# Kernel optimization log

Measured on AMD Instinct MI355X. Metric: run time of the kernel, lower is better.

The kernel has to match this reference:

```python
import jax, jax.numpy as jnp
import numpy as np

B, N, E = 128, 256, 2048
BINS = 16

def _gcn(x, src, dst, W, b):
    # GCNConv with self-loops and symmetric deg^-1/2 normalization (PyG default).
    h = x @ W  # [N, Fout]
    deg = jnp.zeros(x.shape[0], x.dtype).at[dst].add(1.0) + 1.0  # +1 self-loop
    dinv = jax.lax.rsqrt(deg)
    coef = dinv[src] * dinv[dst]  # [E]
    agg = jnp.zeros_like(h).at[dst].add(h[src] * coef[:, None])
    return agg + h / deg[:, None] + b  # self-loop norm = 1/deg

def _gnn(x, ei, W1, b1, W2, b2, W3, b3):
    # x: [B,N,Fin], ei: [B,2,E]. Dropout skipped (eval mode).
    def single(x, ei):
        s, d = ei[0], ei[1]
        h = jax.nn.relu(_gcn(x, s, d, W1, b1))
        h = jax.nn.relu(_gcn(h, s, d, W2, b2))
        return _gcn(h, s, d, W3, b3)
    return jax.vmap(single)(x, ei)

def _att_pool(x, Watt):
    # SimGNN attention pooling; all graphs have exactly N nodes.
    ctx = jnp.tanh((x @ Watt.T).sum(axis=1) / jnp.asarray(N, x.dtype))  # [B,f3]
    scores = jax.nn.sigmoid(jnp.einsum('bnf,bf->bn', x, ctx))  # [B,N]
    return jnp.einsum('bnf,bn->bf', x, scores)  # [B,f3]

def _forward(xq, xc, eq, ec, W1, b1, W2, b2, W3, b3, Watt, ntnW, ntnV, ntnb, fc1W, fc1b, fc2W, fc2b):
    q = _gnn(xq, eq, W1, b1, W2, b2, W3, b3)  # [B,N,f3]
    c = _gnn(xc, ec, W1, b1, W2, b2, W3, b3)
    e1 = _att_pool(q, Watt)
    e2 = _att_pool(c, Watt)
    # NTN: bilinear + linear on concat + bias
    scores = jax.nn.relu(
        jnp.einsum('bi,tij,bj->bt', e1, ntnW, e2)
        + jnp.concatenate([e1, e2], axis=-1) @ ntnV.T
        + ntnb
    )  # [B, tensor_neurons]
    # histogram of all pairwise node-embedding dot products (torch.histc semantics)
    s = jnp.einsum('bnf,bmf->bnm', q, c).ravel()
    lo, hi = s.min(), s.max()
    idx = jnp.clip(jnp.floor((s - lo) / (hi - lo) * BINS).astype(jnp.int32), 0, BINS - 1)
    counts = jnp.zeros(BINS, s.dtype).at[idx].add(1.0)
    h = jax.lax.stop_gradient(counts / counts.sum())
    scores = jnp.concatenate([scores, jnp.broadcast_to(h, (scores.shape[0], BINS))], axis=1)
    scores = jax.nn.relu(scores @ fc1W.T + fc1b)
    p = jax.nn.sigmoid(scores @ fc2W.T + fc2b)  # [B,1]
    return p.squeeze()


def setup_inputs() -> dict:
    key = jax.random.key(0)
    ks = jax.random.split(key, 20)
    Fin, f1, f2, f3, T, BN = 128, 128, 64, 32, 16, 16
    def xav(k, shape):
        fan_in, fan_out = shape[-1], shape[0]
        lim = np.sqrt(6.0 / (fan_in + fan_out))
        return jax.random.uniform(k, shape, jnp.float32, -lim, lim)
    return {
        'xq': jax.random.normal(ks[0], (B, N, Fin), jnp.float32),
        'xc': jax.random.normal(ks[1], (B, N, Fin), jnp.float32),
        'eq': jax.random.randint(ks[2], (B, 2, E), 0, N, jnp.int32),
        'ec': jax.random.randint(ks[3], (B, 2, E), 0, N, jnp.int32),
        'W1': xav(ks[4], (Fin, f1)), 'b1': jnp.zeros((f1,), jnp.float32),
        'W2': xav(ks[5], (f1, f2)), 'b2': jnp.zeros((f2,), jnp.float32),
        'W3': xav(ks[6], (f2, f3)), 'b3': jnp.zeros((f3,), jnp.float32),
        'Watt': xav(ks[7], (f3, f3)),
        'ntnW': xav(ks[8], (T, f3, f3)),
        'ntnV': xav(ks[9], (T, 2 * f3)),
        'ntnb': xav(ks[10], (T, 1)).squeeze(-1),
        'fc1W': xav(ks[11], (BN, T + BINS)), 'fc1b': jnp.zeros((BN,), jnp.float32),
        'fc2W': xav(ks[12], (1, BN)), 'fc2b': jnp.zeros((1,), jnp.float32),
    }


def reference(xq, xc, eq, ec, W1, b1, W2, b2, W3, b3, Watt, ntnW, ntnV, ntnb, fc1W, fc1b, fc2W, fc2b):
    return _forward(xq, xc, eq, ec, W1, b1, W2, b2, W3, b3, Watt, ntnW, ntnV, ntnb, fc1W, fc1b, fc2W, fc2b)
```

## Files before the change

kernel.cpp:

```cpp
#include <hip/hip_runtime.h>
#include <math.h>

#define BB 128
#define NN 256
#define EE 2048
#define BINS 16

typedef unsigned short u16;

__global__ void csr_kernel(const int* __restrict__ eq, const int* __restrict__ ec,
                           int* __restrict__ off, u16* __restrict__ srcs,
                           float* __restrict__ dvsg) {
    int g = blockIdx.x;
    int b = g < BB ? g : g - BB;
    const int* ei = g < BB ? eq : ec;
    int t = threadIdx.x;
    __shared__ int cnt[NN];
    __shared__ int sa[NN], sb[NN];
    __shared__ int cursor[NN];
    cnt[t] = 0;
    __syncthreads();
    const int* src = ei + b * 2 * EE;
    const int* dst = src + EE;
    for (int e = t; e < EE; e += 256) atomicAdd(&cnt[dst[e]], 1);
    __syncthreads();
    dvsg[g * NN + t] = rsqrtf((float)cnt[t] + 1.0f);
    sa[t] = cnt[t];
    __syncthreads();
    int* pin = sa; int* pout = sb;
    for (int d = 1; d < NN; d <<= 1) {
        int v = pin[t];
        if (t >= d) v += pin[t - d];
        pout[t] = v;
        __syncthreads();
        int* tmp = pin; pin = pout; pout = tmp;
    }
    int excl = pin[t] - cnt[t];
    off[g * 257 + t] = excl;
    if (t == 255) off[g * 257 + 256] = EE;
    cursor[t] = excl;
    __syncthreads();
    for (int e = t; e < EE; e += 256) {
        int d = dst[e], s = src[e];
        int pos = atomicAdd(&cursor[d], 1);
        srcs[g * EE + pos] = (u16)s;
    }
}

template<int FIN, int FOUT, bool RELU, int NSPLIT>
__global__ __launch_bounds__(512) void gcn_fused4(
        const float* __restrict__ X0, const float* __restrict__ X1,
        const float* __restrict__ W, const float* __restrict__ bias,
        const int* __restrict__ off, const u16* __restrict__ srcs,
        const float* __restrict__ dvsg, float* __restrict__ OUT) {
    constexpr int CHUNKS = FOUT / 32;
    int blk = blockIdx.x;
    int g = blk % (2 * BB);
    int rest = blk / (2 * BB);
    int cb = (rest % CHUNKS) * 32;
    int half = rest / CHUNKS;
    int t = threadIdx.x;

    __shared__ float uni[NN * 33];
    __shared__ int   eoff[NN + 1];
    __shared__ u16   esrc[EE];
    __shared__ float dvs_s[NN];
    float* xsT = uni;
    float* wt  = uni + 16 * 260;
    float* hT  = uni;

    const float* xg = (g < BB) ? (X0 + (size_t)g * NN * FIN)
                               : (X1 + (size_t)(g - BB) * NN * FIN);
    const int* o = off + g * 257;
    const u16* sr = srcs + (size_t)g * EE;

    for (int i = t; i < EE; i += 512) esrc[i] = sr[i];
    for (int i = t; i <= NN; i += 512) eoff[i] = o[i];
    if (t < NN) dvs_s[t] = dvsg[g * NN + t];

    int l = t & 63;
    int wv = t >> 6;

    float acc[4][4];
#pragma unroll
    for (int i = 0; i < 4; i++)
#pragma unroll
        for (int j = 0; j < 4; j++) acc[i][j] = 0.f;

    int sn = t >> 1, qk = (t & 1) * 8;
    const float* xr = xg + sn * FIN + qk;
    float4 v0 = *(const float4*)xr;
    float4 v1 = *(const float4*)(xr + 4);
    float wreg = W[(t >> 5) * FOUT + cb + (t & 31)];

    for (int k0 = 0; k0 < FIN; k0 += 16) {
        xsT[(qk + 0) * 260 + sn] = v0.x;
        xsT[(qk + 1) * 260 + sn] = v0.y;
        xsT[(qk + 2) * 260 + sn] = v0.z;
        xsT[(qk + 3) * 260 + sn] = v0.w;
        xsT[(qk + 4) * 260 + sn] = v1.x;
        xsT[(qk + 5) * 260 + sn] = v1.y;
        xsT[(qk + 6) * 260 + sn] = v1.z;
        xsT[(qk + 7) * 260 + sn] = v1.w;
        wt[t] = wreg;
        __syncthreads();
        if (k0 + 16 < FIN) {
            xr += 16;
            v0 = *(const float4*)xr;
            v1 = *(const float4*)(xr + 4);
            wreg = W[(k0 + 16 + (t >> 5)) * FOUT + cb + (t & 31)];
        }
#pragma unroll
        for (int k = 0; k < 16; k++) {
            float4 xv = *(const float4*)&xsT[k * 260 + 4 * l];
            float4 wvv = *(const float4*)&wt[k * 32 + 4 * wv];
            acc[0][0] += xv.x * wvv.x; acc[0][1] += xv.x * wvv.y;
            acc[0][2] += xv.x * wvv.z; acc[0][3] += xv.x * wvv.w;
            acc[1][0] += xv.y * wvv.x; acc[1][1] += xv.y * wvv.y;
            acc[1][2] += xv.y * wvv.z; acc[1][3] += xv.y * wvv.w;
            acc[2][0] += xv.z * wvv.x; acc[2][1] += xv.z * wvv.y;
            acc[2][2] += xv.z * wvv.z; acc[2][3] += xv.z * wvv.w;
            acc[3][0] += xv.w * wvv.x; acc[3][1] += xv.w * wvv.y;
            acc[3][2] += xv.w * wvv.z; acc[3][3] += xv.w * wvv.w;
        }
        __syncthreads();
    }
#pragma unroll
    for (int i = 0; i < 4; i++)
#pragma unroll
        for (int j = 0; j < 4; j++)
            hT[(4 * l + i) * 33 + 4 * wv + j] = acc[i][j];
    __syncthreads();

    int c = t & 31, ng = t >> 5;
    float bb_ = bias[cb + c];
    float* outp = OUT + (size_t)g * NN * FOUT;
    constexpr int NSEG = NN / NSPLIT;
    int nlo = half * NSEG, nhi = nlo + NSEG;
    for (int n = nlo + ng; n < nhi; n += 16) {
        int j0 = eoff[n], j1 = eoff[n + 1];
        float dn = dvs_s[n];
        float a = 0.f;
        int j = j0;
        for (; j + 1 < j1; j += 2) {
            int s0 = esrc[j], s1 = esrc[j + 1];
            a += hT[s0 * 33 + c] * (dvs_s[s0] * dn);
            a += hT[s1 * 33 + c] * (dvs_s[s1] * dn);
        }
        if (j < j1) {
            int s0 = esrc[j];
            a += hT[s0 * 33 + c] * (dvs_s[s0] * dn);
        }
        float d0i = 1.0f / ((float)(j1 - j0) + 1.0f);
        float val = a + hT[n * 33 + c] * d0i + bb_;
        if (RELU) val = fmaxf(val, 0.f);
        outp[n * FOUT + cb + c] = val;
    }
}

__global__ void attpool_kernel(const float* __restrict__ X, const float* __restrict__ Watt,
                               float* __restrict__ e) {
    int g = blockIdx.x;
    int t = threadIdx.x;
    __shared__ float xs[NN * 33];
    __shared__ float red[256];
    __shared__ float mean_s[32], ctx_s[32], sc[NN];
    const float* x = X + (size_t)g * NN * 32;
    for (int i = t; i < NN * 32; i += 256) { int n = i >> 5, c = i & 31; xs[n * 33 + c] = x[i]; }
    __syncthreads();
    {
        int c = t & 31, p = t >> 5;
        float s = 0.f;
        for (int n = p * 32; n < (p + 1) * 32; n++) s += xs[n * 33 + c];
        red[t] = s;
    }
    __syncthreads();
    if (t < 32) {
        float m = 0.f;
        for (int p = 0; p < 8; p++) m += red[p * 32 + t];
        mean_s[t] = m / (float)NN;
    }
    __syncthreads();
    if (t < 32) {
        float a = 0.f;
        for (int f = 0; f < 32; f++) a += mean_s[f] * Watt[t * 32 + f];
        ctx_s[t] = tanhf(a);
    }
    __syncthreads();
    {
        float a = 0.f;
        for (int f = 0; f < 32; f++) a += xs[t * 33 + f] * ctx_s[f];
        sc[t] = 1.f / (1.f + expf(-a));
    }
    __syncthreads();
    {
        int c = t & 31, p = t >> 5;
        float s = 0.f;
        for (int n = p * 32; n < (p + 1) * 32; n++) s += xs[n * 33 + c] * sc[n];
        red[t] = s;
    }
    __syncthreads();
    if (t < 32) {
        float s = 0.f;
        for (int p = 0; p < 8; p++) s += red[p * 32 + t];
        e[g * 32 + t] = s;
    }
}

#define PD_STAGE_AND_DOT \
    int blk = blockIdx.x; \
    int b = blk >> 2; \
    int tq = (blk >> 1) & 1, tc = blk & 1; \
    __shared__ float qsT[32 * 132]; \
    __shared__ float csT[32 * 132]; \
    int t = threadIdx.x; \
    { \
        int n = t >> 1, f0 = (t & 1) * 16; \
        const float* qp = Q + ((size_t)b * NN + tq * 128 + n) * 32 + f0; \
        const float* cp = C + ((size_t)b * NN + tc * 128 + n) * 32 + f0; \
        float qa16[16], ca16[16]; \
        *(float4*)&qa16[0]  = *(const float4*)(qp); \
        *(float4*)&qa16[4]  = *(const float4*)(qp + 4); \
        *(float4*)&qa16[8]  = *(const float4*)(qp + 8); \
        *(float4*)&qa16[12] = *(const float4*)(qp + 12); \
        *(float4*)&ca16[0]  = *(const float4*)(cp); \
        *(float4*)&ca16[4]  = *(const float4*)(cp + 4); \
        *(float4*)&ca16[8]  = *(const float4*)(cp + 8); \
        *(float4*)&ca16[12] = *(const float4*)(cp + 12); \
        _Pragma("unroll") \
        for (int m = 0; m < 16; m++) { \
            qsT[(f0 + m) * 132 + n] = qa16[m]; \
            csT[(f0 + m) * 132 + n] = ca16[m]; \
        } \
    } \
    __syncthreads(); \
    int rg = (t >> 4) * 4, cg = (t & 15) * 4; \
    float acc[8][8]; \
    _Pragma("unroll") \
    for (int i = 0; i < 8; i++) \
        _Pragma("unroll") \
        for (int j = 0; j < 8; j++) acc[i][j] = 0.f; \
    _Pragma("unroll 2") \
    for (int f = 0; f < 32; f++) { \
        float4 qa = *(const float4*)&qsT[f * 132 + rg]; \
        float4 qb = *(const float4*)&qsT[f * 132 + 64 + rg]; \
        float4 ca = *(const float4*)&csT[f * 132 + cg]; \
        float4 cb = *(const float4*)&csT[f * 132 + 64 + cg]; \
        float qv[8] = {qa.x, qa.y, qa.z, qa.w, qb.x, qb.y, qb.z, qb.w}; \
        float cv[8] = {ca.x, ca.y, ca.z, ca.w, cb.x, cb.y, cb.z, cb.w}; \
        _Pragma("unroll") \
        for (int i = 0; i < 8; i++) \
            _Pragma("unroll") \
            for (int j = 0; j < 8; j++) acc[i][j] += qv[i] * cv[j]; \
    }

__global__ __launch_bounds__(256, 4) void pairdot_minmax(
        const float* __restrict__ Q, const float* __restrict__ C,
        float* __restrict__ bmin, float* __restrict__ bmax) {
    PD_STAGE_AND_DOT
    float lmin = acc[0][0], lmax = acc[0][0];
#pragma unroll
    for (int i = 0; i < 8; i++)
#pragma unroll
        for (int j = 0; j < 8; j++) {
            lmin = fminf(lmin, acc[i][j]);
            lmax = fmaxf(lmax, acc[i][j]);
        }
    __shared__ float rmin[256], rmax[256];
    rmin[t] = lmin; rmax[t] = lmax;
    __syncthreads();
    for (int s = 128; s > 0; s >>= 1) {
        if (t < s) { rmin[t] = fminf(rmin[t], rmin[t + s]); rmax[t] = fmaxf(rmax[t], rmax[t + s]); }
        __syncthreads();
    }
    if (t == 0) { bmin[blk] = rmin[0]; bmax[blk] = rmax[0]; }
}

__global__ void minmax_kernel(const float* __restrict__ bmin, const float* __restrict__ bmax,
                              float* __restrict__ lohi, float* __restrict__ counts) {
    __shared__ float rmin[256], rmax[256];
    int t = threadIdx.x;
    float lmin = 1e30f, lmax = -1e30f;
    for (int i = t; i < 512; i += 256) { lmin = fminf(lmin, bmin[i]); lmax = fmaxf(lmax, bmax[i]); }
    rmin[t] = lmin; rmax[t] = lmax;
    __syncthreads();
    for (int s = 128; s > 0; s >>= 1) {
        if (t < s) { rmin[t] = fminf(rmin[t], rmin[t + s]); rmax[t] = fmaxf(rmax[t], rmax[t + s]); }
        __syncthreads();
    }
    if (t == 0) { lohi[0] = rmin[0]; lohi[1] = rmax[0]; }
    if (t < BINS) counts[t] = 0.f;
}

__global__ __launch_bounds__(256, 4) void pairdot_hist(
        const float* __restrict__ Q, const float* __restrict__ C,
        const float* __restrict__ lohi, float* __restrict__ counts) {
    PD_STAGE_AND_DOT
    float lo = lohi[0], hi = lohi[1];
    float scale = (float)BINS / (hi - lo);
    int lane = t & 63;
    int cnt = 0;
#pragma unroll
    for (int i = 0; i < 8; i++)
#pragma unroll
        for (int j = 0; j < 8; j++) {
            int idx = (int)floorf((acc[i][j] - lo) * scale);
            idx = min(max(idx, 0), BINS - 1);
            unsigned long long b0 = __ballot((idx & 1) != 0);
            unsigned long long b1 = __ballot((idx & 2) != 0);
            unsigned long long b2 = __ballot((idx & 4) != 0);
            unsigned long long b3 = __ballot((idx & 8) != 0);
            unsigned long long msk = ((lane & 1) ? b0 : ~b0);
            msk &= ((lane & 2) ? b1 : ~b1);
            msk &= ((lane & 4) ? b2 : ~b2);
            msk &= ((lane & 8) ? b3 : ~b3);
            cnt += __popcll(msk);
        }
    __shared__ float wbins[4][BINS];
    int wave = t >> 6;
    if (lane < BINS) wbins[wave][lane] = (float)cnt;
    __syncthreads();
    if (t < BINS) {
        atomicAdd(&counts[t], wbins[0][t] + wbins[1][t] + wbins[2][t] + wbins[3][t]);
    }
}

__global__ void final_kernel(const float* __restrict__ e1, const float* __restrict__ e2,
                             const float* __restrict__ ntnW, const float* __restrict__ ntnV,
                             const float* __restrict__ ntnb, const float* __restrict__ counts,
                             const float* __restrict__ fc1W, const float* __restrict__ fc1b,
                             const float* __restrict__ fc2W, const float* __restrict__ fc2b,
                             float* __restrict__ out) {
    int b = blockIdx.x;
    int t = threadIdx.x;
    __shared__ float a1[32], a2[32], red[256], z[32], u[16];
    if (t < 32) a1[t] = e1[b * 32 + t];
    else if (t < 64) a2[t - 32] = e2[b * 32 + t - 32];
    __syncthreads();
    int tt = t >> 4, g = t & 15;
    float p = 0.f;
#pragma unroll
    for (int ii = 0; ii < 2; ii++) {
        int i = g + 16 * ii;
        float d = 0.f;
        const float* wr = ntnW + (tt * 32 + i) * 32;
        for (int j = 0; j < 32; j++) d += wr[j] * a2[j];
        p += a1[i] * d;
    }
    red[t] = p;
    __syncthreads();
    if (t < 16) {
        float s = 0.f;
        for (int g2 = 0; g2 < 16; g2++) s += red[t * 16 + g2];
        float lin = ntnb[t];
        for (int i = 0; i < 32; i++) lin += ntnV[t * 64 + i] * a1[i];
        for (int i = 0; i < 32; i++) lin += ntnV[t * 64 + 32 + i] * a2[i];
        z[t] = fmaxf(s + lin, 0.f);
    } else if (t < 32) {
        float tot = 0.f;
        for (int i = 0; i < BINS; i++) tot += counts[i];
        z[t] = counts[t - 16] / tot;
    }
    __syncthreads();
    if (t < 16) {
        float a = fc1b[t];
        for (int i = 0; i < 32; i++) a += fc1W[t * 32 + i] * z[i];
        u[t] = fmaxf(a, 0.f);
    }
    __syncthreads();
    if (t == 0) {
        float a = fc2b[0];
        for (int i = 0; i < 16; i++) a += fc2W[i] * u[i];
        out[b] = 1.f / (1.f + expf(-a));
    }
}

extern "C" void kernel_launch(void* const* d_in, const int* in_sizes, int n_in,
                              void* d_out, int out_size, void* d_ws, size_t ws_size,
                              hipStream_t stream) {
    const float* xq   = (const float*)d_in[0];
    const float* xc   = (const float*)d_in[1];
    const int*   eq   = (const int*)d_in[2];
    const int*   ec   = (const int*)d_in[3];
    const float* W1   = (const float*)d_in[4];
    const float* b1   = (const float*)d_in[5];
    const float* W2   = (const float*)d_in[6];
    const float* b2   = (const float*)d_in[7];
    const float* W3   = (const float*)d_in[8];
    const float* b3   = (const float*)d_in[9];
    const float* Watt = (const float*)d_in[10];
    const float* ntnW = (const float*)d_in[11];
    const float* ntnV = (const float*)d_in[12];
    const float* ntnb = (const float*)d_in[13];
    const float* fc1W = (const float*)d_in[14];
    const float* fc1b = (const float*)d_in[15];
    const float* fc2W = (const float*)d_in[16];
    const float* fc2b = (const float*)d_in[17];
    float* out = (float*)d_out;
    float* ws  = (float*)d_ws;

    float* O3   = ws;
    float* e12  = O3 + 2097152;
    float* bmin = e12 + 8192;
    float* bmax = bmin + 2048;
    float* lohi = bmax + 2048;
    float* cntw = lohi + 2;
    int*   off  = (int*)(ws + 2109504);
    u16*   srcs = (u16*)(off + 65792);
    float* dvsg = ws + 2437440;
    float* O1   = ws + 3223872;
    float* O2   = O1 + 8388608;

    float* O3Q = O3;
    float* O3C = O3 + (size_t)BB * NN * 32;
    float* e1w = e12;
    float* e2w = e12 + BB * 32;

    csr_kernel<<<2 * BB, 256, 0, stream>>>(eq, ec, off, srcs, dvsg);

    gcn_fused4<128, 128, true, 1><<<4 * 2 * BB, 512, 0, stream>>>(
        xq, xc, W1, b1, off, srcs, dvsg, O1);
    gcn_fused4<128, 64, true, 1><<<2 * 2 * BB, 512, 0, stream>>>(
        O1, O1 + (size_t)BB * NN * 128, W2, b2, off, srcs, dvsg, O2);
    gcn_fused4<64, 32, false, 2><<<2 * 2 * BB, 512, 0, stream>>>(
        O2, O2 + (size_t)BB * NN * 64, W3, b3, off, srcs, dvsg, O3);

    attpool_kernel<<<2 * BB, 256, 0, stream>>>(O3, Watt, e12);

    pairdot_minmax<<<BB * 4, 256, 0, stream>>>(O3Q, O3C, bmin, bmax);
    minmax_kernel<<<1, 256, 0, stream>>>(bmin, bmax, lohi, cntw);
    pairdot_hist<<<BB * 4, 256, 0, stream>>>(O3Q, O3C, lohi, cntw);

    final_kernel<<<BB, 256, 0, stream>>>(e1w, e2w, ntnW, ntnV, ntnb, cntw,
                                         fc1W, fc1b, fc2W, fc2b, out);
}
```

Before: 299.5 us.

## Precompute per-edge GCN weights, split shared buffers, fold min/max into atomics

The CSR kernel now computes the normalized weight dinv[s]*dinv[d] for each edge and stores it with 32-bit sources. The aggregation loop then reads one precomputed weight instead of two dinv values and a multiply, and uses a software-pipelined loop. The GCN kernel stops aliasing its shared buffers, which raises LDS use and may lower occupancy. The separate min/max reduction kernel is removed: each block does order-preserving encoded atomicMin/atomicMax on the global lo/hi, and the csr kernel initializes lo/hi and the counts, saving one launch.

```diff
diff --git a/kernel.cpp b/kernel.cpp
--- a/kernel.cpp
+++ b/kernel.cpp
@@ -6,25 +6,40 @@
 #define EE 2048
 #define BINS 16
 
-typedef unsigned short u16;
+__device__ __forceinline__ unsigned int fenc(float f) {
+    unsigned int u = __float_as_uint(f);
+    return (u & 0x80000000u) ? ~u : (u | 0x80000000u);
+}
+__device__ __forceinline__ float fdec(unsigned int u) {
+    return (u & 0x80000000u) ? __uint_as_float(u & 0x7FFFFFFFu)
+                             : __uint_as_float(~u);
+}
 
 __global__ void csr_kernel(const int* __restrict__ eq, const int* __restrict__ ec,
-                           int* __restrict__ off, u16* __restrict__ srcs,
-                           float* __restrict__ dvsg) {
+                           int* __restrict__ off, int* __restrict__ srcs,
+                           float* __restrict__ wts,
+                           unsigned int* __restrict__ lohiE,
+                           float* __restrict__ counts) {
     int g = blockIdx.x;
     int b = g < BB ? g : g - BB;
     const int* ei = g < BB ? eq : ec;
     int t = threadIdx.x;
+    if (g == 0) {
+        if (t < BINS) counts[t] = 0.f;
+        if (t == 16) lohiE[0] = 0xFFFFFFFFu;
+        if (t == 17) lohiE[1] = 0u;
+    }
     __shared__ int cnt[NN];
     __shared__ int sa[NN], sb[NN];
     __shared__ int cursor[NN];
+    __shared__ float dvs[NN];
     cnt[t] = 0;
     __syncthreads();
     const int* src = ei + b * 2 * EE;
     const int* dst = src + EE;
     for (int e = t; e < EE; e += 256) atomicAdd(&cnt[dst[e]], 1);
     __syncthreads();
-    dvsg[g * NN + t] = rsqrtf((float)cnt[t] + 1.0f);
+    dvs[t] = rsqrtf((float)cnt[t] + 1.0f);
     sa[t] = cnt[t];
     __syncthreads();
     int* pin = sa; int* pout = sb;
@@ -43,16 +58,17 @@
     for (int e = t; e < EE; e += 256) {
         int d = dst[e], s = src[e];
         int pos = atomicAdd(&cursor[d], 1);
-        srcs[g * EE + pos] = (u16)s;
+        srcs[g * EE + pos] = s;
+        wts[g * EE + pos] = dvs[s] * dvs[d];
     }
 }
 
 template<int FIN, int FOUT, bool RELU, int NSPLIT>
-__global__ __launch_bounds__(512) void gcn_fused4(
+__global__ __launch_bounds__(512) void gcn_fused8(
         const float* __restrict__ X0, const float* __restrict__ X1,
         const float* __restrict__ W, const float* __restrict__ bias,
-        const int* __restrict__ off, const u16* __restrict__ srcs,
-        const float* __restrict__ dvsg, float* __restrict__ OUT) {
+        const int* __restrict__ off, const int* __restrict__ srcs,
+        const float* __restrict__ wts, float* __restrict__ OUT) {
     constexpr int CHUNKS = FOUT / 32;
     int blk = blockIdx.x;
     int g = blk % (2 * BB);
@@ -61,22 +77,21 @@
     int half = rest / CHUNKS;
     int t = threadIdx.x;
 
-    __shared__ float uni[NN * 33];
+    __shared__ float hT[NN * 33];
+    __shared__ float xsT[16 * 260];
+    __shared__ float wt[16 * 32];
     __shared__ int   eoff[NN + 1];
-    __shared__ u16   esrc[EE];
-    __shared__ float dvs_s[NN];
-    float* xsT = uni;
-    float* wt  = uni + 16 * 260;
-    float* hT  = uni;
+    __shared__ int   esrc[EE];
+    __shared__ float ewt[EE];
 
     const float* xg = (g < BB) ? (X0 + (size_t)g * NN * FIN)
                                : (X1 + (size_t)(g - BB) * NN * FIN);
     const int* o = off + g * 257;
-    const u16* sr = srcs + (size_t)g * EE;
-
-    for (int i = t; i < EE; i += 512) esrc[i] = sr[i];
+    const int* sr = srcs + (size_t)g * EE;
+    const float* wg = wts + (size_t)g * EE;
+
+    for (int i = t; i < EE; i += 512) { esrc[i] = sr[i]; ewt[i] = wg[i]; }
     for (int i = t; i <= NN; i += 512) eoff[i] = o[i];
-    if (t < NN) dvs_s[t] = dvsg[g * NN + t];
 
     int l = t & 63;
     int wv = t >> 6;
@@ -139,20 +154,21 @@
     int nlo = half * NSEG, nhi = nlo + NSEG;
     for (int n = nlo + ng; n < nhi; n += 16) {
         int j0 = eoff[n], j1 = eoff[n + 1];
-        float dn = dvs_s[n];
         float a = 0.f;
         int j = j0;
-        for (; j + 1 < j1; j += 2) {
-            int s0 = esrc[j], s1 = esrc[j + 1];
-            a += hT[s0 * 33 + c] * (dvs_s[s0] * dn);
-            a += hT[s1 * 33 + c] * (dvs_s[s1] * dn);
-        }
         if (j < j1) {
             int s0 = esrc[j];
-            a += hT[s0 * 33 + c] * (dvs_s[s0] * dn);
+            float w0 = ewt[j];
+            for (++j; j < j1; ++j) {
+                int s1 = esrc[j];
+                float w1 = ewt[j];
+                a += hT[s0 * 33 + c] * w0;
+                s0 = s1; w0 = w1;
+            }
+            a += hT[s0 * 33 + c] * w0;
         }
-        float d0i = 1.0f / ((float)(j1 - j0) + 1.0f);
-        float val = a + hT[n * 33 + c] * d0i + bb_;
+        float d0 = rsqrtf((float)(j1 - j0) + 1.0f);
+        float val = a + hT[n * 33 + c] * d0 * d0 + bb_;
         if (RELU) val = fmaxf(val, 0.f);
         outp[n * FOUT + cb + c] = val;
     }
@@ -256,7 +272,7 @@
 
 __global__ __launch_bounds__(256, 4) void pairdot_minmax(
         const float* __restrict__ Q, const float* __restrict__ C,
-        float* __restrict__ bmin, float* __restrict__ bmax) {
+        unsigned int* __restrict__ lohiE) {
     PD_STAGE_AND_DOT
     float lmin = acc[0][0], lmax = acc[0][0];
 #pragma unroll
@@ -273,30 +289,17 @@
         if (t < s) { rmin[t] = fminf(rmin[t], rmin[t + s]); rmax[t] = fmaxf(rmax[t], rmax[t + s]); }
         __syncthreads();
     }
-    if (t == 0) { bmin[blk] = rmin[0]; bmax[blk] = rmax[0]; }
-}
-
-__global__ void minmax_kernel(const float* __restrict__ bmin, const float* __restrict__ bmax,
-                              float* __restrict__ lohi, float* __restrict__ counts) {
-    __shared__ float rmin[256], rmax[256];
-    int t = threadIdx.x;
-    float lmin = 1e30f, lmax = -1e30f;
-    for (int i = t; i < 512; i += 256) { lmin = fminf(lmin, bmin[i]); lmax = fmaxf(lmax, bmax[i]); }
-    rmin[t] = lmin; rmax[t] = lmax;
-    __syncthreads();
-    for (int s = 128; s > 0; s >>= 1) {
-        if (t < s) { rmin[t] = fminf(rmin[t], rmin[t + s]); rmax[t] = fmaxf(rmax[t], rmax[t + s]); }
-        __syncthreads();
-    }
-    if (t == 0) { lohi[0] = rmin[0]; lohi[1] = rmax[0]; }
-    if (t < BINS) counts[t] = 0.f;
+    if (t == 0) {
+        atomicMin(&lohiE[0], fenc(rmin[0]));
+        atomicMax(&lohiE[1], fenc(rmax[0]));
+    }
 }
 
 __global__ __launch_bounds__(256, 4) void pairdot_hist(
         const float* __restrict__ Q, const float* __restrict__ C,
-        const float* __restrict__ lohi, float* __restrict__ counts) {
+        const unsigned int* __restrict__ lohiE, float* __restrict__ counts) {
     PD_STAGE_AND_DOT
-    float lo = lohi[0], hi = lohi[1];
+    float lo = fdec(lohiE[0]), hi = fdec(lohiE[1]);
     float scale = (float)BINS / (hi - lo);
     int lane = t & 63;
     int cnt = 0;
@@ -403,11 +406,11 @@
     float* e12  = O3 + 2097152;
     float* bmin = e12 + 8192;
     float* bmax = bmin + 2048;
-    float* lohi = bmax + 2048;
-    float* cntw = lohi + 2;
+    unsigned int* lohiE = (unsigned int*)(bmax + 2048);
+    float* cntw = (float*)(lohiE + 2);
     int*   off  = (int*)(ws + 2109504);
-    u16*   srcs = (u16*)(off + 65792);
-    float* dvsg = ws + 2437440;
+    int*   srcs = off + 65792;
+    float* wts  = (float*)(srcs + 524288);
     float* O1   = ws + 3223872;
     float* O2   = O1 + 8388608;
 
@@ -415,21 +418,21 @@
     float* O3C = O3 + (size_t)BB * NN * 32;
     float* e1w = e12;
     float* e2w = e12 + BB * 32;
-
-    csr_kernel<<<2 * BB, 256, 0, stream>>>(eq, ec, off, srcs, dvsg);
-
-    gcn_fused4<128, 128, true, 1><<<4 * 2 * BB, 512, 0, stream>>>(
-        xq, xc, W1, b1, off, srcs, dvsg, O1);
-    gcn_fused4<128, 64, true, 1><<<2 * 2 * BB, 512, 0, stream>>>(
-        O1, O1 + (size_t)BB * NN * 128, W2, b2, off, srcs, dvsg, O2);
-    gcn_fused4<64, 32, false, 2><<<2 * 2 * BB, 512, 0, stream>>>(
-        O2, O2 + (size_t)BB * NN * 64, W3, b3, off, srcs, dvsg, O3);
+    (void)bmin; (void)bmax;
+
+    csr_kernel<<<2 * BB, 256, 0, stream>>>(eq, ec, off, srcs, wts, lohiE, cntw);
+
+    gcn_fused8<128, 128, true, 1><<<4 * 2 * BB, 512, 0, stream>>>(
+        xq, xc, W1, b1, off, srcs, wts, O1);
+    gcn_fused8<128, 64, true, 1><<<2 * 2 * BB, 512, 0, stream>>>(
+        O1, O1 + (size_t)BB * NN * 128, W2, b2, off, srcs, wts, O2);
+    gcn_fused8<64, 32, false, 2><<<2 * 2 * BB, 512, 0, stream>>>(
+        O2, O2 + (size_t)BB * NN * 64, W3, b3, off, srcs, wts, O3);
 
     attpool_kernel<<<2 * BB, 256, 0, stream>>>(O3, Watt, e12);
 
-    pairdot_minmax<<<BB * 4, 256, 0, stream>>>(O3Q, O3C, bmin, bmax);
-    minmax_kernel<<<1, 256, 0, stream>>>(bmin, bmax, lohi, cntw);
-    pairdot_hist<<<BB * 4, 256, 0, stream>>>(O3Q, O3C, lohi, cntw);
+    pairdot_minmax<<<BB * 4, 256, 0, stream>>>(O3Q, O3C, lohiE);
+    pairdot_hist<<<BB * 4, 256, 0, stream>>>(O3Q, O3C, lohiE, cntw);
 
     final_kernel<<<BB, 256, 0, stream>>>(e1w, e2w, ntnW, ntnV, ntnb, cntw,
                                          fc1W, fc1b, fc2W, fc2b, out);
```

New measurement: 278.9 us (median of 2 runs). -6.9%, faster.
